# Kernel tuning notes

Hardware: AMD Instinct MI355X
Metric: run time of the kernel (lower is better)

## Reference

```python
import jax, jax.numpy as jnp
import numpy as np


def setup_inputs() -> dict:
    key = jax.random.key(0)
    k1, k2, k3 = jax.random.split(key, 3)
    shape = (32, 64, 128, 128)  # B, C, H, W
    out = jax.random.normal(k1, shape, dtype=jnp.float32)
    vals = jax.random.normal(k2, shape, dtype=jnp.float32)
    keep = jax.random.uniform(k3, shape) < 0.1
    target = jnp.where(keep, vals, 0.0).astype(jnp.float32)
    return {"out": out, "target": target}


def reference(out, target):
    # Original loops over every nonzero index of target and sums
    # F.smooth_l1_loss (beta=1, mean over a single scalar == elementwise value).
    # Equivalent fused form: masked elementwise smooth-L1, summed.
    d = jnp.abs(out - target)
    sl1 = jnp.where(d < 1.0, 0.5 * d * d, d - 0.5)
    mask = target != 0.0
    return jnp.sum(jnp.where(mask, sl1, 0.0))
```

## Files before the change

kernel.cpp:

```cpp
#include <hip/hip_runtime.h>


__global__ void zero_out_kernel(float* out) {
    out[0] = 0.0f;
}

__device__ __forceinline__ float sl1_masked(float o, float t) {
    float d = fabsf(o - t);
    float s = (d < 1.0f) ? (0.5f * d * d) : (d - 0.5f);
    return (t != 0.0f) ? s : 0.0f;
}

__global__ __launch_bounds__(256) void sl1_reduce_kernel(
    const float4* __restrict__ o4,
    const float4* __restrict__ t4,
    float* __restrict__ result,
    long long n4)
{
    long long i = (long long)blockIdx.x * blockDim.x + threadIdx.x;
    const long long stride = (long long)gridDim.x * blockDim.x;
    float acc = 0.0f;
    for (; i < n4; i += stride) {
        float4 o = o4[i];
        float4 t = t4[i];
        acc += sl1_masked(o.x, t.x);
        acc += sl1_masked(o.y, t.y);
        acc += sl1_masked(o.z, t.z);
        acc += sl1_masked(o.w, t.w);
    }

    #pragma unroll
    for (int off = 32; off > 0; off >>= 1)
        acc += __shfl_down(acc, off, 64);

    __shared__ float wave_sums[4];
    const int lane = threadIdx.x & 63;
    const int wave = threadIdx.x >> 6;
    if (lane == 0) wave_sums[wave] = acc;
    __syncthreads();

    if (threadIdx.x == 0) {
        float s = wave_sums[0] + wave_sums[1] + wave_sums[2] + wave_sums[3];
        atomicAdd(result, s);
    }
}

extern "C" void kernel_launch(void* const* d_in, const int* in_sizes, int n_in,
                              void* d_out, int out_size, void* d_ws, size_t ws_size,
                              hipStream_t stream) {
    const float* out_p    = (const float*)d_in[0];
    const float* target_p = (const float*)d_in[1];
    float* res = (float*)d_out;

    const long long n = (long long)in_sizes[0];
    const long long n4 = n / 4;

    zero_out_kernel<<<1, 1, 0, stream>>>(res);

    const int block = 256;
    const int grid = 2048;
    sl1_reduce_kernel<<<grid, block, 0, stream>>>(
        (const float4*)out_p, (const float4*)target_p, res, n4);
}
```

Baseline: 279.6 us.

## Replace grid-stride loop with one-shot blocks issuing all loads up front

```diff
diff --git a/kernel.cpp b/kernel.cpp
--- a/kernel.cpp
+++ b/kernel.cpp
@@ -1,9 +1,5 @@
 #include <hip/hip_runtime.h>
 
-
-__global__ void zero_out_kernel(float* out) {
-    out[0] = 0.0f;
-}
 
 __device__ __forceinline__ float sl1_masked(float o, float t) {
     float d = fabsf(o - t);
@@ -17,16 +13,34 @@
     float* __restrict__ result,
     long long n4)
 {
-    long long i = (long long)blockIdx.x * blockDim.x + threadIdx.x;
-    const long long stride = (long long)gridDim.x * blockDim.x;
+    const long long base = (long long)blockIdx.x * 1024 + threadIdx.x;
+
+    float4 o[4], t[4];
+    if (base + 768 < n4) {
+        #pragma unroll
+        for (int k = 0; k < 4; ++k) {
+            o[k] = o4[base + (long long)k * 256];
+            t[k] = t4[base + (long long)k * 256];
+        }
+    } else {
+        #pragma unroll
+        for (int k = 0; k < 4; ++k) {
+            long long idx = base + (long long)k * 256;
+            if (idx < n4) { o[k] = o4[idx]; t[k] = t4[idx]; }
+            else {
+                o[k] = make_float4(0.f, 0.f, 0.f, 0.f);
+                t[k] = make_float4(0.f, 0.f, 0.f, 0.f);
+            }
+        }
+    }
+
     float acc = 0.0f;
-    for (; i < n4; i += stride) {
-        float4 o = o4[i];
-        float4 t = t4[i];
-        acc += sl1_masked(o.x, t.x);
-        acc += sl1_masked(o.y, t.y);
-        acc += sl1_masked(o.z, t.z);
-        acc += sl1_masked(o.w, t.w);
+    #pragma unroll
+    for (int k = 0; k < 4; ++k) {
+        acc += sl1_masked(o[k].x, t[k].x);
+        acc += sl1_masked(o[k].y, t[k].y);
+        acc += sl1_masked(o[k].z, t[k].z);
+        acc += sl1_masked(o[k].w, t[k].w);
     }
 
     #pragma unroll
@@ -52,13 +66,14 @@
     const float* target_p = (const float*)d_in[1];
     float* res = (float*)d_out;
 
-    const long long n = (long long)in_sizes[0];
+    const long long n  = (long long)in_sizes[0];
     const long long n4 = n / 4;
 
-    zero_out_kernel<<<1, 1, 0, stream>>>(res);
+    hipMemsetAsync(res, 0, sizeof(float), stream);
 
     const int block = 256;
-    const int grid = 2048;
+    const long long per_block = 1024;
+    const int grid = (int)((n4 + per_block - 1) / per_block);
     sl1_reduce_kernel<<<grid, block, 0, stream>>>(
         (const float4*)out_p, (const float4*)target_p, res, n4);
 }
```

Measured after the change: 297.7 us. 1.07x slower.

## Use two-pass reduction with nontemporal prefetched loads and larger grid

Applied to the files above, without the earlier changes.

```diff
diff --git a/kernel.cpp b/kernel.cpp
--- a/kernel.cpp
+++ b/kernel.cpp
@@ -1,9 +1,7 @@
 #include <hip/hip_runtime.h>
 
 
-__global__ void zero_out_kernel(float* out) {
-    out[0] = 0.0f;
-}
+typedef float v4f __attribute__((ext_vector_type(4)));
 
 __device__ __forceinline__ float sl1_masked(float o, float t) {
     float d = fabsf(o - t);
@@ -11,54 +9,76 @@
     return (t != 0.0f) ? s : 0.0f;
 }
 
-__global__ __launch_bounds__(256) void sl1_reduce_kernel(
-    const float4* __restrict__ o4,
-    const float4* __restrict__ t4,
-    float* __restrict__ result,
-    long long n4)
-{
-    long long i = (long long)blockIdx.x * blockDim.x + threadIdx.x;
-    const long long stride = (long long)gridDim.x * blockDim.x;
-    float acc = 0.0f;
-    for (; i < n4; i += stride) {
-        float4 o = o4[i];
-        float4 t = t4[i];
-        acc += sl1_masked(o.x, t.x);
-        acc += sl1_masked(o.y, t.y);
-        acc += sl1_masked(o.z, t.z);
-        acc += sl1_masked(o.w, t.w);
-    }
+__device__ __forceinline__ float sl1_v4(v4f o, v4f t) {
+    return sl1_masked(o.x, t.x) + sl1_masked(o.y, t.y) +
+           sl1_masked(o.z, t.z) + sl1_masked(o.w, t.w);
+}
 
+__device__ __forceinline__ float block_reduce(float acc) {
     #pragma unroll
     for (int off = 32; off > 0; off >>= 1)
         acc += __shfl_down(acc, off, 64);
-
     __shared__ float wave_sums[4];
     const int lane = threadIdx.x & 63;
     const int wave = threadIdx.x >> 6;
     if (lane == 0) wave_sums[wave] = acc;
     __syncthreads();
+    return wave_sums[0] + wave_sums[1] + wave_sums[2] + wave_sums[3];
+}
 
-    if (threadIdx.x == 0) {
-        float s = wave_sums[0] + wave_sums[1] + wave_sums[2] + wave_sums[3];
-        atomicAdd(result, s);
+__global__ __launch_bounds__(256) void sl1_partial_kernel(
+    const v4f* __restrict__ o4,
+    const v4f* __restrict__ t4,
+    float* __restrict__ partials,
+    long long n4)
+{
+    const long long stride = (long long)gridDim.x * blockDim.x;
+    long long i = (long long)blockIdx.x * blockDim.x + threadIdx.x;
+
+    float acc = 0.0f;
+    if (i < n4) {
+        v4f o_cur = __builtin_nontemporal_load(&o4[i]);
+        v4f t_cur = __builtin_nontemporal_load(&t4[i]);
+        for (long long j = i + stride; j < n4; j += stride) {
+            v4f o_nxt = __builtin_nontemporal_load(&o4[j]);
+            v4f t_nxt = __builtin_nontemporal_load(&t4[j]);
+            acc += sl1_v4(o_cur, t_cur);
+            o_cur = o_nxt;
+            t_cur = t_nxt;
+        }
+        acc += sl1_v4(o_cur, t_cur);
     }
+
+    float s = block_reduce(acc);
+    if (threadIdx.x == 0) partials[blockIdx.x] = s;
+}
+
+__global__ __launch_bounds__(256) void sl1_final_kernel(
+    const float* __restrict__ partials,
+    float* __restrict__ result,
+    int n)
+{
+    float acc = 0.0f;
+    for (int i = threadIdx.x; i < n; i += 256)
+        acc += partials[i];
+    float s = block_reduce(acc);
+    if (threadIdx.x == 0) result[0] = s;
 }
 
 extern "C" void kernel_launch(void* const* d_in, const int* in_sizes, int n_in,
                               void* d_out, int out_size, void* d_ws, size_t ws_size,
                               hipStream_t stream) {
-    const float* out_p    = (const float*)d_in[0];
-    const float* target_p = (const float*)d_in[1];
-    float* res = (float*)d_out;
+    const v4f* o4 = (const v4f*)d_in[0];
+    const v4f* t4 = (const v4f*)d_in[1];
+    float* res      = (float*)d_out;
+    float* partials = (float*)d_ws;
 
-    const long long n = (long long)in_sizes[0];
+    const long long n  = (long long)in_sizes[0];
     const long long n4 = n / 4;
 
-    zero_out_kernel<<<1, 1, 0, stream>>>(res);
+    const int block = 256;
+    const int grid  = 4096;
 
-    const int block = 256;
-    const int grid = 2048;
-    sl1_reduce_kernel<<<grid, block, 0, stream>>>(
-        (const float4*)out_p, (const float4*)target_p, res, n4);
+    sl1_partial_kernel<<<grid, block, 0, stream>>>(o4, t4, partials, n4);
+    sl1_final_kernel<<<1, block, 0, stream>>>(partials, res, grid);
 }
```

Result: faster. 254.6 us (-8.9%).
